# Kernel tuning notes

Hardware: AMD Instinct MI355X
Metric: run time of the kernel (lower is better)

Reference implementation:

```python
import jax, jax.numpy as jnp
import numpy as np

N_NODES = 50000
N_EDGES = 800000
F_IN = 128
HEADS = 4
HEAD_DIM = 32  # hidden_size // heads
HIDDEN = HEADS * HEAD_DIM
N_GRAPHS = 64
LEAKY_SLOPE = 0.01
EPS_LN = 1e-5


def setup_inputs() -> dict:
    key = jax.random.key(0)
    ks = jax.random.split(key, 12)
    x = jax.random.normal(ks[0], (N_NODES, F_IN), dtype=jnp.float32)
    edge_index = jax.random.randint(ks[1], (2, N_EDGES), 0, N_NODES, dtype=jnp.int64)
    batch = jnp.sort(jax.random.randint(ks[2], (N_NODES,), 0, N_GRAPHS, dtype=jnp.int64))
    s = 1.0 / np.sqrt(F_IN).astype(np.float32)
    Wq = jax.random.normal(ks[3], (F_IN, HIDDEN), dtype=jnp.float32) * s
    bq = jnp.zeros((HIDDEN,), jnp.float32)
    Wk = jax.random.normal(ks[4], (F_IN, HIDDEN), dtype=jnp.float32) * s
    bk = jnp.zeros((HIDDEN,), jnp.float32)
    Wv = jax.random.normal(ks[5], (F_IN, HIDDEN), dtype=jnp.float32) * s
    bv = jnp.zeros((HIDDEN,), jnp.float32)
    Ws = jax.random.normal(ks[6], (F_IN, HIDDEN), dtype=jnp.float32) * s  # root/skip lin
    bs = jnp.zeros((HIDDEN,), jnp.float32)
    ln_w = jnp.ones((HIDDEN,), jnp.float32)
    ln_b = jnp.zeros((HIDDEN,), jnp.float32)
    return {"x": x, "edge_index": edge_index, "batch": batch,
            "Wq": Wq, "bq": bq, "Wk": Wk, "bk": bk, "Wv": Wv, "bv": bv,
            "Ws": Ws, "bs": bs, "ln_w": ln_w, "ln_b": ln_b}


def reference(x, edge_index, batch, Wq, bq, Wk, bk, Wv, bv, Ws, bs, ln_w, ln_b):
    N = x.shape[0]
    src, dst = edge_index[0], edge_index[1]  # message j(src) -> i(dst)
    q = (x @ Wq + bq).reshape(N, HEADS, HEAD_DIM)
    k = (x @ Wk + bk).reshape(N, HEADS, HEAD_DIM)
    v = (x @ Wv + bv).reshape(N, HEADS, HEAD_DIM)
    # per-edge attention logits [E, H]
    alpha = jnp.einsum('ehc,ehc->eh', q[dst], k[src]) / jnp.sqrt(jnp.float32(HEAD_DIM))
    # scatter-softmax over incoming edges of each destination node
    m = jax.ops.segment_max(alpha, dst, num_segments=N)
    m = jnp.where(jnp.isfinite(m), m, 0.0)  # empty segments -> -inf; neutralize
    ex = jnp.exp(alpha - m[dst])
    denom = jax.ops.segment_sum(ex, dst, num_segments=N)
    attn = ex / (denom[dst] + 1e-16)
    # scatter-add aggregation of weighted values, concat heads
    out = jax.ops.segment_sum(attn[:, :, None] * v[src], dst, num_segments=N)
    out = out.reshape(N, HIDDEN) + x @ Ws + bs  # root/skip connection
    # PyG graph-mode LayerNorm: normalize over all nodes+channels of each graph
    cnt = jax.ops.segment_sum(jnp.ones((N,), out.dtype), batch, num_segments=N_GRAPHS)
    norm = jnp.maximum(cnt, 1.0) * HIDDEN
    mean = jax.ops.segment_sum(out.sum(-1), batch, num_segments=N_GRAPHS) / norm
    outc = out - mean[batch][:, None]
    var = jax.ops.segment_sum((outc * outc).sum(-1), batch, num_segments=N_GRAPHS) / norm
    y = outc / jnp.sqrt(var + EPS_LN)[batch][:, None]
    y = y * ln_w + ln_b
    y = jnp.where(y > 0, y, LEAKY_SLOPE * y)  # LeakyReLU
    return (y, attn)
```

## Files before the change

kernel.cpp:

```cpp
#include <hip/hip_runtime.h>
#include <hip/hip_fp16.h>

constexpr int N_NODES = 50000;
constexpr int N_EDGES = 800000;
constexpr int HIDDEN  = 128;
constexpr float RSQRT_D = 0.17677669529663687f;
constexpr int Y_SIZE = N_NODES * HIDDEN;
constexpr int M_PAD  = 50048;
constexpr int SCAN_BLOCKS = 196;
constexpr int XCVT_BLOCKS = (M_PAD * 16) / 256;
constexpr int HIST_BLOCKS = N_EDGES / 256;
constexpr int NORM_BLOCKS = (N_EDGES * 4) / 256;
constexpr int STAT_BLOCKS = (N_NODES + 31) / 32;

constexpr size_t OFF_Q      = 0;
constexpr size_t OFF_K      = 6400000;
constexpr size_t OFF_S      = 19200000;
constexpr size_t OFF_DENOM  = 25600000;
constexpr size_t OFF_GSUM   = 25800000;
constexpr size_t OFF_GSQ    = 25800064;
constexpr size_t OFF_GCNT   = 25800128;
constexpr size_t OFF_DEG    = 25800192;
constexpr size_t OFF_OFFS   = 25850192;
constexpr size_t OFF_CURSOR = 25900224;
constexpr size_t OFF_CSR    = 25950224;
constexpr size_t OFF_PART   = 27550224;

typedef __attribute__((ext_vector_type(8))) short bf16x8;
typedef __attribute__((ext_vector_type(4))) float f32x4;

__device__ __forceinline__ short f2bf(float f) {
    unsigned u = __float_as_uint(f);
    unsigned r = (u + 0x7fff + ((u >> 16) & 1)) >> 16;
    return (short)r;
}

__device__ __forceinline__ void gload_lds16(const void* g, void* l) {
    __builtin_amdgcn_global_load_lds(
        (const __attribute__((address_space(1))) void*)g,
        (__attribute__((address_space(3))) void*)l, 16, 0, 0);
}

__global__ __launch_bounds__(256) void k_prep(
    const float* __restrict__ x,
    const float* __restrict__ Wq, const float* __restrict__ Wk,
    const float* __restrict__ Wv, const float* __restrict__ Wsm,
    const int* __restrict__ dst,
    short* __restrict__ xs, short* __restrict__ wt, int* __restrict__ deg)
{
    int b = blockIdx.x;
    if (b < XCVT_BLOCKS) {
        int tid = b * 256 + threadIdx.x;
        int row = tid >> 4, ci = tid & 15;
        short o[8];
        if (row < N_NODES) {
            float4 a = *(const float4*)&x[(size_t)row * 128 + ci * 8];
            float4 bb = *(const float4*)&x[(size_t)row * 128 + ci * 8 + 4];
            o[0] = f2bf(a.x); o[1] = f2bf(a.y); o[2] = f2bf(a.z); o[3] = f2bf(a.w);
            o[4] = f2bf(bb.x); o[5] = f2bf(bb.y); o[6] = f2bf(bb.z); o[7] = f2bf(bb.w);
        } else {
            #pragma unroll
            for (int j = 0; j < 8; ++j) o[j] = 0;
        }
        int cs = ci ^ (row & 7);
        *(int4*)&xs[(size_t)row * 128 + cs * 8] = *(int4*)o;
    } else if (b < XCVT_BLOCKS + 32) {
        int tid = (b - XCVT_BLOCKS) * 256 + threadIdx.x;
        int mat = tid >> 11, n = (tid >> 4) & 127, kg = tid & 15;
        const float* W = (mat == 0) ? Wq : (mat == 1) ? Wk : (mat == 2) ? Wv : Wsm;
        short o[8];
        #pragma unroll
        for (int j = 0; j < 8; ++j) o[j] = f2bf(W[(kg * 8 + j) * 128 + n]);
        int cs = kg ^ (n & 7);
        *(int4*)&wt[mat * 16384 + n * 128 + cs * 8] = *(int4*)o;
    } else {
        int e = (b - XCVT_BLOCKS - 32) * 256 + threadIdx.x;
        atomicAdd(&deg[dst[e]], 1);
    }
}

__global__ __launch_bounds__(256) void k_mm(
    const short* __restrict__ xs, const short* __restrict__ wt,
    const float* __restrict__ bq, const float* __restrict__ bk,
    const float* __restrict__ bv, const float* __restrict__ bs,
    __half* __restrict__ qb, __half* __restrict__ kv, __half* __restrict__ sb)
{
    __shared__ __align__(16) char As[32768];
    __shared__ __align__(16) char Bs[32768];
    const int t = threadIdx.x, lane = t & 63, wv = t >> 6;
    const int m0 = blockIdx.x * 128;
    const int wm = wv >> 1, wn = wv & 1;

    const char* gA = (const char*)xs + (size_t)m0 * 256;
    #pragma unroll
    for (int i = 0; i < 8; ++i) {
        int chunk = wv * 8 + i;
        gload_lds16(gA + chunk * 1024 + lane * 16, As + chunk * 1024);
        gload_lds16((const char*)wt + chunk * 1024 + lane * 16, Bs + chunk * 1024);
    }
    __syncthreads();

    bf16x8 af[4][4];
    #pragma unroll
    for (int ks = 0; ks < 4; ++ks) {
        const int cbase = ks * 64 + ((lane >> 4) << 4);
        #pragma unroll
        for (int mf = 0; mf < 4; ++mf) {
            int mr = wm * 64 + mf * 16 + (lane & 15);
            af[ks][mf] = *(const bf16x8*)(As + mr * 256 + (cbase ^ ((mr & 7) << 4)));
        }
    }

    const float* Bbs[4] = {bq, bk, bv, bs};
    #pragma unroll
    for (int mat = 0; mat < 4; ++mat) {
        f32x4 acc[4][4];
        #pragma unroll
        for (int nf = 0; nf < 4; ++nf) {
            float bc = Bbs[mat][wn * 64 + nf * 16 + (lane & 15)];
            #pragma unroll
            for (int mf = 0; mf < 4; ++mf) acc[mf][nf] = (f32x4){bc, bc, bc, bc};
        }
        #pragma unroll
        for (int ks = 0; ks < 4; ++ks) {
            bf16x8 bfr[4];
            const int cbase = ks * 64 + ((lane >> 4) << 4);
            #pragma unroll
            for (int nf = 0; nf < 4; ++nf) {
                int nc = wn * 64 + nf * 16 + (lane & 15);
                bfr[nf] = *(const bf16x8*)(Bs + nc * 256 + (cbase ^ ((nc & 7) << 4)));
            }
            #pragma unroll
            for (int mf = 0; mf < 4; ++mf)
                #pragma unroll
                for (int nf = 0; nf < 4; ++nf)
                    acc[mf][nf] = __builtin_amdgcn_mfma_f32_16x16x32_bf16(
                        af[ks][mf], bfr[nf], acc[mf][nf], 0, 0, 0);
        }
        __syncthreads();
        if (mat < 3) {
            const char* gB = (const char*)wt + (mat + 1) * 32768;
            #pragma unroll
            for (int i = 0; i < 8; ++i) {
                int chunk = wv * 8 + i;
                gload_lds16(gB + chunk * 1024 + lane * 16, Bs + chunk * 1024);
            }
        }
        __half* base = (mat == 0) ? qb : (mat == 1) ? kv : (mat == 2) ? (kv + 128) : sb;
        const int rs = (mat == 1 || mat == 2) ? 256 : 128;
        const int colbase = wn * 64 + (lane & 15);
        #pragma unroll
        for (int mf = 0; mf < 4; ++mf) {
            int rowb = m0 + wm * 64 + mf * 16 + ((lane >> 4) << 2);
            #pragma unroll
            for (int nf = 0; nf < 4; ++nf) {
                int col = colbase + nf * 16;
                #pragma unroll
                for (int r = 0; r < 4; ++r) {
                    int node = rowb + r;
                    if (node < N_NODES)
                        base[(size_t)node * rs + col] = __float2half_rn(acc[mf][nf][r]);
                }
            }
        }
        __syncthreads();
    }
}

__global__ __launch_bounds__(256) void k_scan1(const int* __restrict__ deg,
                                               int* __restrict__ part)
{
    const int t = threadIdx.x;
    int idx = blockIdx.x * 256 + t;
    int v = (idx < N_NODES) ? deg[idx] : 0;
    #pragma unroll
    for (int o = 1; o < 64; o <<= 1) v += __shfl_xor(v, o);
    __shared__ int wsum[4];
    if ((t & 63) == 0) wsum[t >> 6] = v;
    __syncthreads();
    if (t == 0) part[blockIdx.x] = wsum[0] + wsum[1] + wsum[2] + wsum[3];
}

__global__ __launch_bounds__(256) void k_scan2(int* __restrict__ part)
{
    __shared__ int buf[256];
    const int t = threadIdx.x;
    int v = (t < SCAN_BLOCKS) ? part[t] : 0;
    buf[t] = v;
    __syncthreads();
    for (int o = 1; o < 256; o <<= 1) {
        int tmp = (t >= o) ? buf[t - o] : 0;
        __syncthreads();
        buf[t] += tmp;
        __syncthreads();
    }
    if (t < SCAN_BLOCKS) part[t] = buf[t] - v;
}

__global__ __launch_bounds__(256) void k_scan3(const int* __restrict__ deg,
                                               const int* __restrict__ part,
                                               int* __restrict__ offs,
                                               int* __restrict__ cursor)
{
    const int t = threadIdx.x;
    const int idx = blockIdx.x * 256 + t;
    const int lane = t & 63, w = t >> 6;
    int v = (idx < N_NODES) ? deg[idx] : 0;
    int inc = v;
    #pragma unroll
    for (int o = 1; o < 64; o <<= 1) {
        int nb = __shfl_up(inc, o);
        if (lane >= o) inc += nb;
    }
    __shared__ int wsum[4];
    if (lane == 63) wsum[w] = inc;
    __syncthreads();
    int wbase = 0;
    #pragma unroll
    for (int i = 0; i < 4; ++i) if (i < w) wbase += wsum[i];
    int excl = part[blockIdx.x] + wbase + inc - v;
    if (idx < N_NODES) {
        offs[idx] = excl;
        cursor[idx] = excl;
    }
    if (idx == 0) offs[N_NODES] = N_EDGES;
}

__global__ __launch_bounds__(256) void k_scatter(
    const int* __restrict__ src, const int* __restrict__ dst,
    int* __restrict__ cursor, int2* __restrict__ csr)
{
    int e = blockIdx.x * 256 + threadIdx.x;
    int d = dst[e];
    int pos = atomicAdd(&cursor[d], 1);
    csr[pos] = make_int2(src[e], e);
}

__global__ __launch_bounds__(256) void k_fused(
    const __half* __restrict__ qb, const __half* __restrict__ kv,
    const __half* __restrict__ sb,
    const int* __restrict__ offs, const int2* __restrict__ csr,
    float* __restrict__ exbuf, float* __restrict__ denom,
    float* __restrict__ outb)
{
    const int t = threadIdx.x;
    const int lane = t & 63;
    const int n = blockIdx.x * 4 + (t >> 6);
    const int begin = offs[n], end = offs[n + 1];
    const int cl  = lane & 15;
    const int qtr = lane >> 4;
    const int h   = cl >> 2;

    const __half2* qp = (const __half2*)(qb + (size_t)n * 128 + cl * 8);
    float2 qf[4];
    #pragma unroll
    for (int j = 0; j < 4; ++j) qf[j] = __half22float2(qp[j]);

    float acc[8] = {0.f, 0.f, 0.f, 0.f, 0.f, 0.f, 0.f, 0.f};
    float dsum = 0.f;
    int i = begin;
    for (; i + 8 <= end; i += 8) {
        const int2 c0 = csr[i + qtr];
        const int2 c1 = csr[i + 4 + qtr];
        const __half2* k0 = (const __half2*)(kv + (size_t)c0.x * 256 + cl * 8);
        const __half2* k1 = (const __half2*)(kv + (size_t)c1.x * 256 + cl * 8);
        __half2 ka[4], kb2[4], va[4], vb2[4];
        #pragma unroll
        for (int j = 0; j < 4; ++j) { ka[j] = k0[j]; va[j] = k0[64 + j]; }
        #pragma unroll
        for (int j = 0; j < 4; ++j) { kb2[j] = k1[j]; vb2[j] = k1[64 + j]; }
        float p0 = 0.f, p1 = 0.f;
        #pragma unroll
        for (int j = 0; j < 4; ++j) {
            float2 f0 = __half22float2(ka[j]), f1 = __half22float2(kb2[j]);
            p0 += qf[j].x * f0.x + qf[j].y * f0.y;
            p1 += qf[j].x * f1.x + qf[j].y * f1.y;
        }
        p0 += __shfl_xor(p0, 1);  p1 += __shfl_xor(p1, 1);
        p0 += __shfl_xor(p0, 2);  p1 += __shfl_xor(p1, 2);
        const float ex0 = __expf(p0 * RSQRT_D);
        const float ex1 = __expf(p1 * RSQRT_D);
        dsum += ex0 + ex1;
        #pragma unroll
        for (int j = 0; j < 4; ++j) {
            float2 f0 = __half22float2(va[j]), f1 = __half22float2(vb2[j]);
            acc[2*j]   += ex0 * f0.x + ex1 * f1.x;
            acc[2*j+1] += ex0 * f0.y + ex1 * f1.y;
        }
        if ((lane & 3) == 0) {
            exbuf[c0.y * 4 + h] = ex0;
            exbuf[c1.y * 4 + h] = ex1;
        }
    }
    for (; i < end; i += 4) {
        const int eIdx = i + qtr;
        const bool act = eIdx < end;
        const int2 c0 = csr[act ? eIdx : end - 1];
        const __half2* k0 = (const __half2*)(kv + (size_t)c0.x * 256 + cl * 8);
        __half2 ka[4], va[4];
        #pragma unroll
        for (int j = 0; j < 4; ++j) { ka[j] = k0[j]; va[j] = k0[64 + j]; }
        float p0 = 0.f;
        #pragma unroll
        for (int j = 0; j < 4; ++j) {
            float2 f0 = __half22float2(ka[j]);
            p0 += qf[j].x * f0.x + qf[j].y * f0.y;
        }
        p0 += __shfl_xor(p0, 1);
        p0 += __shfl_xor(p0, 2);
        const float ex0 = act ? __expf(p0 * RSQRT_D) : 0.f;
        dsum += ex0;
        #pragma unroll
        for (int j = 0; j < 4; ++j) {
            float2 f0 = __half22float2(va[j]);
            acc[2*j]   += ex0 * f0.x;
            acc[2*j+1] += ex0 * f0.y;
        }
        if (((lane & 3) == 0) && act) exbuf[c0.y * 4 + h] = ex0;
    }
    dsum += __shfl_xor(dsum, 16);
    dsum += __shfl_xor(dsum, 32);
    #pragma unroll
    for (int j = 0; j < 8; ++j) {
        acc[j] += __shfl_xor(acc[j], 16);
        acc[j] += __shfl_xor(acc[j], 32);
    }
    if (lane < 16) {
        if ((lane & 3) == 0) denom[n * 4 + h] = dsum;
        const float rdn = 1.f / (dsum + 1e-16f);
        const __half2* sp = (const __half2*)(sb + (size_t)n * 128 + cl * 8);
        float o[8];
        #pragma unroll
        for (int j = 0; j < 4; ++j) {
            float2 sf = __half22float2(sp[j]);
            o[2*j]   = acc[2*j]   * rdn + sf.x;
            o[2*j+1] = acc[2*j+1] * rdn + sf.y;
        }
        *(float4*)&outb[(size_t)n * 128 + cl * 8]     = make_float4(o[0], o[1], o[2], o[3]);
        *(float4*)&outb[(size_t)n * 128 + cl * 8 + 4] = make_float4(o[4], o[5], o[6], o[7]);
    }
}

__global__ __launch_bounds__(256) void k_post(
    float* __restrict__ attn, const float* __restrict__ denom,
    const int* __restrict__ dst,
    const float* __restrict__ out, const int* __restrict__ batch,
    float* __restrict__ gsum, float* __restrict__ gsq, int* __restrict__ gcnt)
{
    const int b = blockIdx.x;
    if (b < NORM_BLOCKS) {
        int idx = b * 256 + threadIdx.x;
        int e = idx >> 2, h = idx & 3;
        attn[idx] = attn[idx] / (denom[dst[e] * 4 + h] + 1e-16f);
        return;
    }
    __shared__ float nsum[32], nsq[32];
    __shared__ int   ngr[32];
    const int t = threadIdx.x;
    const int nl = t >> 3, part = t & 7;
    const int n = (b - NORM_BLOCKS) * 32 + nl;
    float lsum = 0.f, lsq = 0.f;
    if (n < N_NODES) {
        size_t base = (size_t)n * 128 + part * 16;
        #pragma unroll
        for (int i = 0; i < 4; ++i) {
            float4 o = *(const float4*)&out[base + i * 4];
            lsum += o.x + o.y + o.z + o.w;
            lsq  += o.x * o.x + o.y * o.y + o.z * o.z + o.w * o.w;
        }
    }
    #pragma unroll
    for (int o = 1; o < 8; o <<= 1) {
        lsum += __shfl_xor(lsum, o);
        lsq  += __shfl_xor(lsq, o);
    }
    if (part == 0) { nsum[nl] = lsum; nsq[nl] = lsq; ngr[nl] = (n < N_NODES) ? batch[n] : -1; }
    __syncthreads();
    if (t == 0) {
        float acc = 0.f, accq = 0.f; int cg = ngr[0], cnt = 0;
        for (int i = 0; i < 32; ++i) {
            int g = ngr[i];
            if (g != cg) {
                if (cg >= 0) { atomicAdd(&gsum[cg], acc); atomicAdd(&gsq[cg], accq);
                               atomicAdd(&gcnt[cg], cnt); }
                acc = 0.f; accq = 0.f; cnt = 0; cg = g;
            }
            acc += nsum[i]; accq += nsq[i]; ++cnt;
        }
        if (cg >= 0) { atomicAdd(&gsum[cg], acc); atomicAdd(&gsq[cg], accq);
                       atomicAdd(&gcnt[cg], cnt); }
    }
}

__global__ __launch_bounds__(256) void k_final(
    const float* __restrict__ out, const int* __restrict__ batch,
    const float* __restrict__ gsum, const float* __restrict__ gsq,
    const int* __restrict__ gcnt,
    const float* __restrict__ lnw, const float* __restrict__ lnb,
    float* __restrict__ y)
{
    int idx = blockIdx.x * 256 + threadIdx.x;
    int n = idx >> 7, c = idx & 127;
    int g = batch[n];
    float norm = fmaxf((float)gcnt[g], 1.f) * 128.f;
    float mean = gsum[g] / norm;
    float var  = gsq[g] / norm - mean * mean;
    float inv  = rsqrtf(var + 1e-5f);
    float val  = (out[idx] - mean) * inv * lnw[c] + lnb[c];
    y[idx] = val > 0.f ? val : 0.01f * val;
}

extern "C" void kernel_launch(void* const* d_in, const int* in_sizes, int n_in,
                              void* d_out, int out_size, void* d_ws, size_t ws_size,
                              hipStream_t stream)
{
    (void)in_sizes; (void)n_in; (void)out_size; (void)ws_size;
    const float* x    = (const float*)d_in[0];
    const int*   ei   = (const int*)  d_in[1];
    const int*   batch= (const int*)  d_in[2];
    const float* Wq   = (const float*)d_in[3];
    const float* bq   = (const float*)d_in[4];
    const float* Wk   = (const float*)d_in[5];
    const float* bk   = (const float*)d_in[6];
    const float* Wv   = (const float*)d_in[7];
    const float* bv   = (const float*)d_in[8];
    const float* Wsm  = (const float*)d_in[9];
    const float* bs   = (const float*)d_in[10];
    const float* lnw  = (const float*)d_in[11];
    const float* lnb  = (const float*)d_in[12];

    float* outp = (float*)d_out;
    float* ws   = (float*)d_ws;

    const int* srcI = ei;
    const int* dstI = ei + N_EDGES;

    __half* qb      = (__half*)(ws + OFF_Q);
    __half* kv      = (__half*)(ws + OFF_K);
    __half* sb      = (__half*)(ws + OFF_S);
    float*  denom   = ws + OFF_DENOM;
    short*  wt      = (short*)(ws + OFF_DENOM);
    float*  gsum    = ws + OFF_GSUM;
    float*  gsq     = ws + OFF_GSQ;
    int*    gcnt    = (int*)(ws + OFF_GCNT);
    int*    deg     = (int*)(ws + OFF_DEG);
    int*    offs    = (int*)(ws + OFF_OFFS);
    int*    cursor  = (int*)(ws + OFF_CURSOR);
    int2*   csr     = (int2*)(ws + OFF_CSR);
    int*    partArr = (int*)(ws + OFF_PART);

    float* outb  = outp;
    short* x_swz = (short*)outp;
    float* attn  = outp + Y_SIZE;

    hipMemsetAsync(gsum, 0, (size_t)(192 + N_NODES) * sizeof(float), stream);

    k_prep<<<XCVT_BLOCKS + 32 + HIST_BLOCKS, 256, 0, stream>>>(
        x, Wq, Wk, Wv, Wsm, dstI, x_swz, wt, deg);
    k_mm<<<M_PAD / 128, 256, 0, stream>>>(x_swz, wt, bq, bk, bv, bs, qb, kv, sb);

    k_scan1<<<SCAN_BLOCKS, 256, 0, stream>>>(deg, partArr);
    k_scan2<<<1, 256, 0, stream>>>(partArr);
    k_scan3<<<SCAN_BLOCKS, 256, 0, stream>>>(deg, partArr, offs, cursor);
    k_scatter<<<N_EDGES / 256, 256, 0, stream>>>(srcI, dstI, cursor, csr);
    k_fused<<<N_NODES / 4, 256, 0, stream>>>(qb, kv, sb, offs, csr,
                                             attn, denom, outb);
    k_post<<<NORM_BLOCKS + STAT_BLOCKS, 256, 0, stream>>>(
        attn, denom, dstI, outb, batch, gsum, gsq, gcnt);
    k_final<<<Y_SIZE / 256, 256, 0, stream>>>(outb, batch, gsum, gsq, gcnt,
                                              lnw, lnb, outp);
}
```

Before: 230.8 us.

## Fuse x bf16 conversion into GEMM, merge scan kernels, store ex in CSR order

Converts x to swizzled bf16 directly inside the GEMM's LDS staging instead of in a separate prep pass, so the intermediate bf16 copy of x is never written or read back. Folds the single-block partial scan into each k_scan3 block, removing one launch at the cost of redundant per-block work. The CSR now stores only source indices plus a per-edge position array. The fused kernel writes exp values contiguously in CSR order, and the post kernel gathers them through pos, so the scattered stores move from the hot aggregation kernel to the normalization pass.

```diff
diff --git a/kernel.cpp b/kernel.cpp
--- a/kernel.cpp
+++ b/kernel.cpp
@@ -8,7 +8,6 @@
 constexpr int Y_SIZE = N_NODES * HIDDEN;
 constexpr int M_PAD  = 50048;
 constexpr int SCAN_BLOCKS = 196;
-constexpr int XCVT_BLOCKS = (M_PAD * 16) / 256;
 constexpr int HIST_BLOCKS = N_EDGES / 256;
 constexpr int NORM_BLOCKS = (N_EDGES * 4) / 256;
 constexpr int STAT_BLOCKS = (N_NODES + 31) / 32;
@@ -16,6 +15,7 @@
 constexpr size_t OFF_Q      = 0;
 constexpr size_t OFF_K      = 6400000;
 constexpr size_t OFF_S      = 19200000;
+constexpr size_t OFF_EXC    = 22400000;
 constexpr size_t OFF_DENOM  = 25600000;
 constexpr size_t OFF_GSUM   = 25800000;
 constexpr size_t OFF_GSQ    = 25800064;
@@ -24,6 +24,7 @@
 constexpr size_t OFF_OFFS   = 25850192;
 constexpr size_t OFF_CURSOR = 25900224;
 constexpr size_t OFF_CSR    = 25950224;
+constexpr size_t OFF_POS    = 26750224;
 constexpr size_t OFF_PART   = 27550224;
 
 typedef __attribute__((ext_vector_type(8))) short bf16x8;
@@ -42,30 +43,14 @@
 }
 
 __global__ __launch_bounds__(256) void k_prep(
-    const float* __restrict__ x,
     const float* __restrict__ Wq, const float* __restrict__ Wk,
     const float* __restrict__ Wv, const float* __restrict__ Wsm,
     const int* __restrict__ dst,
-    short* __restrict__ xs, short* __restrict__ wt, int* __restrict__ deg)
+    short* __restrict__ wt, int* __restrict__ deg)
 {
     int b = blockIdx.x;
-    if (b < XCVT_BLOCKS) {
+    if (b < 32) {
         int tid = b * 256 + threadIdx.x;
-        int row = tid >> 4, ci = tid & 15;
-        short o[8];
-        if (row < N_NODES) {
-            float4 a = *(const float4*)&x[(size_t)row * 128 + ci * 8];
-            float4 bb = *(const float4*)&x[(size_t)row * 128 + ci * 8 + 4];
-            o[0] = f2bf(a.x); o[1] = f2bf(a.y); o[2] = f2bf(a.z); o[3] = f2bf(a.w);
-            o[4] = f2bf(bb.x); o[5] = f2bf(bb.y); o[6] = f2bf(bb.z); o[7] = f2bf(bb.w);
-        } else {
-            #pragma unroll
-            for (int j = 0; j < 8; ++j) o[j] = 0;
-        }
-        int cs = ci ^ (row & 7);
-        *(int4*)&xs[(size_t)row * 128 + cs * 8] = *(int4*)o;
-    } else if (b < XCVT_BLOCKS + 32) {
-        int tid = (b - XCVT_BLOCKS) * 256 + threadIdx.x;
         int mat = tid >> 11, n = (tid >> 4) & 127, kg = tid & 15;
         const float* W = (mat == 0) ? Wq : (mat == 1) ? Wk : (mat == 2) ? Wv : Wsm;
         short o[8];
@@ -74,13 +59,13 @@
         int cs = kg ^ (n & 7);
         *(int4*)&wt[mat * 16384 + n * 128 + cs * 8] = *(int4*)o;
     } else {
-        int e = (b - XCVT_BLOCKS - 32) * 256 + threadIdx.x;
+        int e = (b - 32) * 256 + threadIdx.x;
         atomicAdd(&deg[dst[e]], 1);
     }
 }
 
 __global__ __launch_bounds__(256) void k_mm(
-    const short* __restrict__ xs, const short* __restrict__ wt,
+    const float* __restrict__ x, const short* __restrict__ wt,
     const float* __restrict__ bq, const float* __restrict__ bk,
     const float* __restrict__ bv, const float* __restrict__ bs,
     __half* __restrict__ qb, __half* __restrict__ kv, __half* __restrict__ sb)
@@ -91,12 +76,28 @@
     const int m0 = blockIdx.x * 128;
     const int wm = wv >> 1, wn = wv & 1;
 
-    const char* gA = (const char*)xs + (size_t)m0 * 256;
     #pragma unroll
     for (int i = 0; i < 8; ++i) {
         int chunk = wv * 8 + i;
-        gload_lds16(gA + chunk * 1024 + lane * 16, As + chunk * 1024);
         gload_lds16((const char*)wt + chunk * 1024 + lane * 16, Bs + chunk * 1024);
+    }
+    #pragma unroll
+    for (int j = 0; j < 8; ++j) {
+        int idx = t + 256 * j;
+        int row = idx >> 4, ci = idx & 15;
+        int gr = m0 + row;
+        short o[8];
+        if (gr < N_NODES) {
+            float4 a = *(const float4*)&x[(size_t)gr * 128 + ci * 8];
+            float4 bb = *(const float4*)&x[(size_t)gr * 128 + ci * 8 + 4];
+            o[0] = f2bf(a.x); o[1] = f2bf(a.y); o[2] = f2bf(a.z); o[3] = f2bf(a.w);
+            o[4] = f2bf(bb.x); o[5] = f2bf(bb.y); o[6] = f2bf(bb.z); o[7] = f2bf(bb.w);
+        } else {
+            #pragma unroll
+            for (int j2 = 0; j2 < 8; ++j2) o[j2] = 0;
+        }
+        int cs = ci ^ (row & 7);
+        *(int4*)(As + row * 256 + cs * 16) = *(int4*)o;
     }
     __syncthreads();
 
@@ -181,28 +182,25 @@
     if (t == 0) part[blockIdx.x] = wsum[0] + wsum[1] + wsum[2] + wsum[3];
 }
 
-__global__ __launch_bounds__(256) void k_scan2(int* __restrict__ part)
-{
-    __shared__ int buf[256];
-    const int t = threadIdx.x;
-    int v = (t < SCAN_BLOCKS) ? part[t] : 0;
-    buf[t] = v;
-    __syncthreads();
-    for (int o = 1; o < 256; o <<= 1) {
-        int tmp = (t >= o) ? buf[t - o] : 0;
-        __syncthreads();
-        buf[t] += tmp;
-        __syncthreads();
-    }
-    if (t < SCAN_BLOCKS) part[t] = buf[t] - v;
-}
-
 __global__ __launch_bounds__(256) void k_scan3(const int* __restrict__ deg,
                                                const int* __restrict__ part,
                                                int* __restrict__ offs,
                                                int* __restrict__ cursor)
 {
+    __shared__ int pbuf[256];
+    __shared__ int wsum[4];
     const int t = threadIdx.x;
+    int pv = (t < SCAN_BLOCKS) ? part[t] : 0;
+    pbuf[t] = pv;
+    __syncthreads();
+    for (int o = 1; o < 256; o <<= 1) {
+        int tmp = (t >= o) ? pbuf[t - o] : 0;
+        __syncthreads();
+        pbuf[t] += tmp;
+        __syncthreads();
+    }
+    const int bbase = (blockIdx.x == 0) ? 0 : pbuf[blockIdx.x - 1];
+
     const int idx = blockIdx.x * 256 + t;
     const int lane = t & 63, w = t >> 6;
     int v = (idx < N_NODES) ? deg[idx] : 0;
@@ -212,13 +210,12 @@
         int nb = __shfl_up(inc, o);
         if (lane >= o) inc += nb;
     }
-    __shared__ int wsum[4];
     if (lane == 63) wsum[w] = inc;
     __syncthreads();
     int wbase = 0;
     #pragma unroll
     for (int i = 0; i < 4; ++i) if (i < w) wbase += wsum[i];
-    int excl = part[blockIdx.x] + wbase + inc - v;
+    int excl = bbase + wbase + inc - v;
     if (idx < N_NODES) {
         offs[idx] = excl;
         cursor[idx] = excl;
@@ -228,19 +225,20 @@
 
 __global__ __launch_bounds__(256) void k_scatter(
     const int* __restrict__ src, const int* __restrict__ dst,
-    int* __restrict__ cursor, int2* __restrict__ csr)
+    int* __restrict__ cursor, int* __restrict__ csr_src, int* __restrict__ pos)
 {
     int e = blockIdx.x * 256 + threadIdx.x;
     int d = dst[e];
-    int pos = atomicAdd(&cursor[d], 1);
-    csr[pos] = make_int2(src[e], e);
+    int p = atomicAdd(&cursor[d], 1);
+    csr_src[p] = src[e];
+    pos[e] = p;
 }
 
 __global__ __launch_bounds__(256) void k_fused(
     const __half* __restrict__ qb, const __half* __restrict__ kv,
     const __half* __restrict__ sb,
-    const int* __restrict__ offs, const int2* __restrict__ csr,
-    float* __restrict__ exbuf, float* __restrict__ denom,
+    const int* __restrict__ offs, const int* __restrict__ csr_src,
+    float* __restrict__ exc, float* __restrict__ denom,
     float* __restrict__ outb)
 {
     const int t = threadIdx.x;
@@ -260,10 +258,10 @@
     float dsum = 0.f;
     int i = begin;
     for (; i + 8 <= end; i += 8) {
-        const int2 c0 = csr[i + qtr];
-        const int2 c1 = csr[i + 4 + qtr];
-        const __half2* k0 = (const __half2*)(kv + (size_t)c0.x * 256 + cl * 8);
-        const __half2* k1 = (const __half2*)(kv + (size_t)c1.x * 256 + cl * 8);
+        const int s0 = csr_src[i + qtr];
+        const int s1 = csr_src[i + 4 + qtr];
+        const __half2* k0 = (const __half2*)(kv + (size_t)s0 * 256 + cl * 8);
+        const __half2* k1 = (const __half2*)(kv + (size_t)s1 * 256 + cl * 8);
         __half2 ka[4], kb2[4], va[4], vb2[4];
         #pragma unroll
         for (int j = 0; j < 4; ++j) { ka[j] = k0[j]; va[j] = k0[64 + j]; }
@@ -288,15 +286,15 @@
             acc[2*j+1] += ex0 * f0.y + ex1 * f1.y;
         }
         if ((lane & 3) == 0) {
-            exbuf[c0.y * 4 + h] = ex0;
-            exbuf[c1.y * 4 + h] = ex1;
+            exc[(i + qtr) * 4 + h]     = ex0;
+            exc[(i + 4 + qtr) * 4 + h] = ex1;
         }
     }
     for (; i < end; i += 4) {
         const int eIdx = i + qtr;
         const bool act = eIdx < end;
-        const int2 c0 = csr[act ? eIdx : end - 1];
-        const __half2* k0 = (const __half2*)(kv + (size_t)c0.x * 256 + cl * 8);
+        const int s0 = csr_src[act ? eIdx : end - 1];
+        const __half2* k0 = (const __half2*)(kv + (size_t)s0 * 256 + cl * 8);
         __half2 ka[4], va[4];
         #pragma unroll
         for (int j = 0; j < 4; ++j) { ka[j] = k0[j]; va[j] = k0[64 + j]; }
@@ -316,7 +314,7 @@
             acc[2*j]   += ex0 * f0.x;
             acc[2*j+1] += ex0 * f0.y;
         }
-        if (((lane & 3) == 0) && act) exbuf[c0.y * 4 + h] = ex0;
+        if (((lane & 3) == 0) && act) exc[eIdx * 4 + h] = ex0;
     }
     dsum += __shfl_xor(dsum, 16);
     dsum += __shfl_xor(dsum, 32);
@@ -342,7 +340,8 @@
 }
 
 __global__ __launch_bounds__(256) void k_post(
-    float* __restrict__ attn, const float* __restrict__ denom,
+    float* __restrict__ attn, const float* __restrict__ exc,
+    const int* __restrict__ pos, const float* __restrict__ denom,
     const int* __restrict__ dst,
     const float* __restrict__ out, const int* __restrict__ batch,
     float* __restrict__ gsum, float* __restrict__ gsq, int* __restrict__ gcnt)
@@ -351,7 +350,8 @@
     if (b < NORM_BLOCKS) {
         int idx = b * 256 + threadIdx.x;
         int e = idx >> 2, h = idx & 3;
-        attn[idx] = attn[idx] / (denom[dst[e] * 4 + h] + 1e-16f);
+        int p = pos[e];
+        attn[idx] = exc[p * 4 + h] / (denom[dst[e] * 4 + h] + 1e-16f);
         return;
     }
     __shared__ float nsum[32], nsq[32];
@@ -438,6 +438,7 @@
     __half* qb      = (__half*)(ws + OFF_Q);
     __half* kv      = (__half*)(ws + OFF_K);
     __half* sb      = (__half*)(ws + OFF_S);
+    float*  exc     = ws + OFF_EXC;
     float*  denom   = ws + OFF_DENOM;
     short*  wt      = (short*)(ws + OFF_DENOM);
     float*  gsum    = ws + OFF_GSUM;
@@ -446,27 +447,25 @@
     int*    deg     = (int*)(ws + OFF_DEG);
     int*    offs    = (int*)(ws + OFF_OFFS);
     int*    cursor  = (int*)(ws + OFF_CURSOR);
-    int2*   csr     = (int2*)(ws + OFF_CSR);
+    int*    csr_src = (int*)(ws + OFF_CSR);
+    int*    pos     = (int*)(ws + OFF_POS);
     int*    partArr = (int*)(ws + OFF_PART);
 
-    float* outb  = outp;
-    short* x_swz = (short*)outp;
-    float* attn  = outp + Y_SIZE;
+    float* outb = outp;
+    float* attn = outp + Y_SIZE;
 
     hipMemsetAsync(gsum, 0, (size_t)(192 + N_NODES) * sizeof(float), stream);
 
-    k_prep<<<XCVT_BLOCKS + 32 + HIST_BLOCKS, 256, 0, stream>>>(
-        x, Wq, Wk, Wv, Wsm, dstI, x_swz, wt, deg);
-    k_mm<<<M_PAD / 128, 256, 0, stream>>>(x_swz, wt, bq, bk, bv, bs, qb, kv, sb);
+    k_prep<<<32 + HIST_BLOCKS, 256, 0, stream>>>(Wq, Wk, Wv, Wsm, dstI, wt, deg);
+    k_mm<<<M_PAD / 128, 256, 0, stream>>>(x, wt, bq, bk, bv, bs, qb, kv, sb);
 
     k_scan1<<<SCAN_BLOCKS, 256, 0, stream>>>(deg, partArr);
-    k_scan2<<<1, 256, 0, stream>>>(partArr);
     k_scan3<<<SCAN_BLOCKS, 256, 0, stream>>>(deg, partArr, offs, cursor);
-    k_scatter<<<N_EDGES / 256, 256, 0, stream>>>(srcI, dstI, cursor, csr);
-    k_fused<<<N_NODES / 4, 256, 0, stream>>>(qb, kv, sb, offs, csr,
-                                             attn, denom, outb);
+    k_scatter<<<N_EDGES / 256, 256, 0, stream>>>(srcI, dstI, cursor, csr_src, pos);
+    k_fused<<<N_NODES / 4, 256, 0, stream>>>(qb, kv, sb, offs, csr_src,
+                                             exc, denom, outb);
     k_post<<<NORM_BLOCKS + STAT_BLOCKS, 256, 0, stream>>>(
-        attn, denom, dstI, outb, batch, gsum, gsq, gcnt);
+        attn, exc, pos, denom, dstI, outb, batch, gsum, gsq, gcnt);
     k_final<<<Y_SIZE / 256, 256, 0, stream>>>(outb, batch, gsum, gsq, gcnt,
                                               lnw, lnb, outp);
 }
```

Measured after the change: 236.2 us. 2.3% more time.

## Fuse attention normalization into edge aggregation kernel and merge scan passes

Applied to the files above, without the earlier changes.

The fused attention kernel now writes unnormalized exp values in CSR order to a scratch buffer. At the end of each node it normalizes them by the per-head denominators and scatters the final attention to edge order. This removes the separate normalization pass, which re-read attn, dst and denom for every edge. The single-block middle scan is folded into the third scan kernel, with every block redundantly scanning the 196 partial sums, to drop one launch. In exchange the kernel gains extra scratch traffic and scattered float4 stores indexed by edge id.

```diff
diff --git a/kernel.cpp b/kernel.cpp
--- a/kernel.cpp
+++ b/kernel.cpp
@@ -10,13 +10,13 @@
 constexpr int SCAN_BLOCKS = 196;
 constexpr int XCVT_BLOCKS = (M_PAD * 16) / 256;
 constexpr int HIST_BLOCKS = N_EDGES / 256;
-constexpr int NORM_BLOCKS = (N_EDGES * 4) / 256;
 constexpr int STAT_BLOCKS = (N_NODES + 31) / 32;
 
 constexpr size_t OFF_Q      = 0;
 constexpr size_t OFF_K      = 6400000;
 constexpr size_t OFF_S      = 19200000;
-constexpr size_t OFF_DENOM  = 25600000;
+constexpr size_t OFF_EXC    = 22400000;
+constexpr size_t OFF_WT     = 25600000;
 constexpr size_t OFF_GSUM   = 25800000;
 constexpr size_t OFF_GSQ    = 25800064;
 constexpr size_t OFF_GCNT   = 25800128;
@@ -181,28 +181,25 @@
     if (t == 0) part[blockIdx.x] = wsum[0] + wsum[1] + wsum[2] + wsum[3];
 }
 
-__global__ __launch_bounds__(256) void k_scan2(int* __restrict__ part)
-{
-    __shared__ int buf[256];
-    const int t = threadIdx.x;
-    int v = (t < SCAN_BLOCKS) ? part[t] : 0;
-    buf[t] = v;
-    __syncthreads();
-    for (int o = 1; o < 256; o <<= 1) {
-        int tmp = (t >= o) ? buf[t - o] : 0;
-        __syncthreads();
-        buf[t] += tmp;
-        __syncthreads();
-    }
-    if (t < SCAN_BLOCKS) part[t] = buf[t] - v;
-}
-
 __global__ __launch_bounds__(256) void k_scan3(const int* __restrict__ deg,
                                                const int* __restrict__ part,
                                                int* __restrict__ offs,
                                                int* __restrict__ cursor)
 {
+    __shared__ int pbuf[256];
+    __shared__ int wsum[4];
     const int t = threadIdx.x;
+    int pv = (t < SCAN_BLOCKS) ? part[t] : 0;
+    pbuf[t] = pv;
+    __syncthreads();
+    for (int o = 1; o < 256; o <<= 1) {
+        int tmp = (t >= o) ? pbuf[t - o] : 0;
+        __syncthreads();
+        pbuf[t] += tmp;
+        __syncthreads();
+    }
+    const int bbase = (blockIdx.x == 0) ? 0 : pbuf[blockIdx.x - 1];
+
     const int idx = blockIdx.x * 256 + t;
     const int lane = t & 63, w = t >> 6;
     int v = (idx < N_NODES) ? deg[idx] : 0;
@@ -212,13 +209,12 @@
         int nb = __shfl_up(inc, o);
         if (lane >= o) inc += nb;
     }
-    __shared__ int wsum[4];
     if (lane == 63) wsum[w] = inc;
     __syncthreads();
     int wbase = 0;
     #pragma unroll
     for (int i = 0; i < 4; ++i) if (i < w) wbase += wsum[i];
-    int excl = part[blockIdx.x] + wbase + inc - v;
+    int excl = bbase + wbase + inc - v;
     if (idx < N_NODES) {
         offs[idx] = excl;
         cursor[idx] = excl;
@@ -232,15 +228,15 @@
 {
     int e = blockIdx.x * 256 + threadIdx.x;
     int d = dst[e];
-    int pos = atomicAdd(&cursor[d], 1);
-    csr[pos] = make_int2(src[e], e);
+    int p = atomicAdd(&cursor[d], 1);
+    csr[p] = make_int2(src[e], e);
 }
 
 __global__ __launch_bounds__(256) void k_fused(
     const __half* __restrict__ qb, const __half* __restrict__ kv,
     const __half* __restrict__ sb,
     const int* __restrict__ offs, const int2* __restrict__ csr,
-    float* __restrict__ exbuf, float* __restrict__ denom,
+    float* __restrict__ exc, float* __restrict__ attn,
     float* __restrict__ outb)
 {
     const int t = threadIdx.x;
@@ -260,10 +256,10 @@
     float dsum = 0.f;
     int i = begin;
     for (; i + 8 <= end; i += 8) {
-        const int2 c0 = csr[i + qtr];
-        const int2 c1 = csr[i + 4 + qtr];
-        const __half2* k0 = (const __half2*)(kv + (size_t)c0.x * 256 + cl * 8);
-        const __half2* k1 = (const __half2*)(kv + (size_t)c1.x * 256 + cl * 8);
+        const int s0 = csr[i + qtr].x;
+        const int s1 = csr[i + 4 + qtr].x;
+        const __half2* k0 = (const __half2*)(kv + (size_t)s0 * 256 + cl * 8);
+        const __half2* k1 = (const __half2*)(kv + (size_t)s1 * 256 + cl * 8);
         __half2 ka[4], kb2[4], va[4], vb2[4];
         #pragma unroll
         for (int j = 0; j < 4; ++j) { ka[j] = k0[j]; va[j] = k0[64 + j]; }
@@ -288,15 +284,15 @@
             acc[2*j+1] += ex0 * f0.y + ex1 * f1.y;
         }
         if ((lane & 3) == 0) {
-            exbuf[c0.y * 4 + h] = ex0;
-            exbuf[c1.y * 4 + h] = ex1;
+            exc[(i + qtr) * 4 + h]     = ex0;
+            exc[(i + 4 + qtr) * 4 + h] = ex1;
         }
     }
     for (; i < end; i += 4) {
         const int eIdx = i + qtr;
         const bool act = eIdx < end;
-        const int2 c0 = csr[act ? eIdx : end - 1];
-        const __half2* k0 = (const __half2*)(kv + (size_t)c0.x * 256 + cl * 8);
+        const int s0 = csr[act ? eIdx : end - 1].x;
+        const __half2* k0 = (const __half2*)(kv + (size_t)s0 * 256 + cl * 8);
         __half2 ka[4], va[4];
         #pragma unroll
         for (int j = 0; j < 4; ++j) { ka[j] = k0[j]; va[j] = k0[64 + j]; }
@@ -316,7 +312,7 @@
             acc[2*j]   += ex0 * f0.x;
             acc[2*j+1] += ex0 * f0.y;
         }
-        if (((lane & 3) == 0) && act) exbuf[c0.y * 4 + h] = ex0;
+        if (((lane & 3) == 0) && act) exc[eIdx * 4 + h] = ex0;
     }
     dsum += __shfl_xor(dsum, 16);
     dsum += __shfl_xor(dsum, 32);
@@ -325,8 +321,12 @@
         acc[j] += __shfl_xor(acc[j], 16);
         acc[j] += __shfl_xor(acc[j], 32);
     }
+    const float rd0 = 1.f / (__shfl(dsum, 0)  + 1e-16f);
+    const float rd1 = 1.f / (__shfl(dsum, 4)  + 1e-16f);
+    const float rd2 = 1.f / (__shfl(dsum, 8)  + 1e-16f);
+    const float rd3 = 1.f / (__shfl(dsum, 12) + 1e-16f);
+
     if (lane < 16) {
-        if ((lane & 3) == 0) denom[n * 4 + h] = dsum;
         const float rdn = 1.f / (dsum + 1e-16f);
         const __half2* sp = (const __half2*)(sb + (size_t)n * 128 + cl * 8);
         float o[8];
@@ -339,26 +339,24 @@
         *(float4*)&outb[(size_t)n * 128 + cl * 8]     = make_float4(o[0], o[1], o[2], o[3]);
         *(float4*)&outb[(size_t)n * 128 + cl * 8 + 4] = make_float4(o[4], o[5], o[6], o[7]);
     }
-}
-
-__global__ __launch_bounds__(256) void k_post(
-    float* __restrict__ attn, const float* __restrict__ denom,
-    const int* __restrict__ dst,
+
+    for (int slot = begin + lane; slot < end; slot += 64) {
+        const int eid = csr[slot].y;
+        float4 e4 = *(const float4*)&exc[slot * 4];
+        ((float4*)attn)[eid] = make_float4(e4.x * rd0, e4.y * rd1,
+                                           e4.z * rd2, e4.w * rd3);
+    }
+}
+
+__global__ __launch_bounds__(256) void k_stats(
     const float* __restrict__ out, const int* __restrict__ batch,
     float* __restrict__ gsum, float* __restrict__ gsq, int* __restrict__ gcnt)
 {
-    const int b = blockIdx.x;
-    if (b < NORM_BLOCKS) {
-        int idx = b * 256 + threadIdx.x;
-        int e = idx >> 2, h = idx & 3;
-        attn[idx] = attn[idx] / (denom[dst[e] * 4 + h] + 1e-16f);
-        return;
-    }
     __shared__ float nsum[32], nsq[32];
     __shared__ int   ngr[32];
     const int t = threadIdx.x;
     const int nl = t >> 3, part = t & 7;
-    const int n = (b - NORM_BLOCKS) * 32 + nl;
+    const int n = blockIdx.x * 32 + nl;
     float lsum = 0.f, lsq = 0.f;
     if (n < N_NODES) {
         size_t base = (size_t)n * 128 + part * 16;
@@ -438,8 +436,8 @@
     __half* qb      = (__half*)(ws + OFF_Q);
     __half* kv      = (__half*)(ws + OFF_K);
     __half* sb      = (__half*)(ws + OFF_S);
-    float*  denom   = ws + OFF_DENOM;
-    short*  wt      = (short*)(ws + OFF_DENOM);
+    float*  exc     = ws + OFF_EXC;
+    short*  wt      = (short*)(ws + OFF_WT);
     float*  gsum    = ws + OFF_GSUM;
     float*  gsq     = ws + OFF_GSQ;
     int*    gcnt    = (int*)(ws + OFF_GCNT);
@@ -460,13 +458,11 @@
     k_mm<<<M_PAD / 128, 256, 0, stream>>>(x_swz, wt, bq, bk, bv, bs, qb, kv, sb);
 
     k_scan1<<<SCAN_BLOCKS, 256, 0, stream>>>(deg, partArr);
-    k_scan2<<<1, 256, 0, stream>>>(partArr);
     k_scan3<<<SCAN_BLOCKS, 256, 0, stream>>>(deg, partArr, offs, cursor);
     k_scatter<<<N_EDGES / 256, 256, 0, stream>>>(srcI, dstI, cursor, csr);
     k_fused<<<N_NODES / 4, 256, 0, stream>>>(qb, kv, sb, offs, csr,
-                                             attn, denom, outb);
-    k_post<<<NORM_BLOCKS + STAT_BLOCKS, 256, 0, stream>>>(
-        attn, denom, dstI, outb, batch, gsum, gsq, gcnt);
+                                             exc, attn, outb);
+    k_stats<<<STAT_BLOCKS, 256, 0, stream>>>(outb, batch, gsum, gsq, gcnt);
     k_final<<<Y_SIZE / 256, 256, 0, stream>>>(outb, batch, gsum, gsq, gcnt,
                                               lnw, lnb, outp);
 }
```

Result: no change. 227.2 us (-1.6%).
